# Kernel tuning notes

Measured on AMD Instinct MI355X. Metric: run time of the kernel, lower is better.

The kernel has to match this reference:

```python
import jax, jax.numpy as jnp
import numpy as np

N = 100_000   # nodes
E = 1_600_000 # edges (COO, directed as given)
D = 128       # input feature dim
H = 128       # hidden dim
L = 3         # layers


def setup_inputs() -> dict:
    key = jax.random.key(0)
    ks = jax.random.split(key, 2 + 2 * L)
    x = jax.random.normal(ks[0], (N, D), dtype=jnp.float32)
    edge_index = jax.random.randint(ks[1], (2, E), 0, N, dtype=jnp.int32)
    inp = {"x": x, "edge_index": edge_index}
    dims = [(D, H), (H, H), (H, H)]
    for i, (fi, fo) in enumerate(dims):
        scale = 1.0 / np.sqrt(fi)
        inp[f"W{i}"] = jax.random.uniform(ks[2 + 2 * i], (fi, fo), jnp.float32, -scale, scale)
        inp[f"b{i}"] = jax.random.uniform(ks[3 + 2 * i], (fo,), jnp.float32, -scale, scale)
    return inp


def reference(x, edge_index, W0, b0, W1, b1, W2, b2):
    n = x.shape[0]
    src, dst = edge_index[0], edge_index[1]
    # GCNConv default: add self-loops, symmetric D^{-1/2}(A+I)D^{-1/2} normalization
    loop = jnp.arange(n, dtype=edge_index.dtype)
    src = jnp.concatenate([src, loop])
    dst = jnp.concatenate([dst, loop])
    ones = jnp.ones(src.shape[0], dtype=x.dtype)
    deg = jax.ops.segment_sum(ones, dst, num_segments=n)          # [N]
    dinv = jnp.where(deg > 0, jax.lax.rsqrt(deg), 0.0)            # deg^{-1/2}, inf->0
    norm = dinv[src] * dinv[dst]                                  # [E+N]

    def gcn_conv(h, W, b):
        h = h @ W                                  # linear transform first (PyG order)
        msg = h[src] * norm[:, None]               # gather + scale, [E+N, H]
        return jax.ops.segment_sum(msg, dst, num_segments=n) + b

    for W, b in ((W0, b0), (W1, b1), (W2, b2)):
        x = jax.nn.relu(gcn_conv(x, W, b))
    return x
```

## Files before the change

kernel.cpp:

```cpp
#include <hip/hip_runtime.h>
#include <hip/hip_bf16.h>

#define TPB 256

typedef short s8v __attribute__((ext_vector_type(8)));
typedef float f4v __attribute__((ext_vector_type(4)));
typedef _Float16 h8v __attribute__((ext_vector_type(8)));

#define PB 128
#define BSHIFT 10
#define BSPAN 1024
#define PCHUNK 4096
#define WBLK 192

__device__ __forceinline__ unsigned short bf16_rne(float v) {
    unsigned int u = __float_as_uint(v);
    u += 0x7fffu + ((u >> 16) & 1u);
    return (unsigned short)(u >> 16);
}
__device__ __forceinline__ void split_bf16(float v, unsigned short& hi, unsigned short& lo) {
    hi = bf16_rne(v);
    float hf = __uint_as_float((unsigned int)hi << 16);
    lo = bf16_rne(v - hf);
}


__global__ __launch_bounds__(256) void bhist_wsplit_kernel(const int* __restrict__ dst, int E,
                                                           int* __restrict__ bsize,
                                                           const float* __restrict__ W0,
                                                           const float* __restrict__ W1,
                                                           const float* __restrict__ W2,
                                                           unsigned short* __restrict__ Whi,
                                                           unsigned short* __restrict__ Wlo) {
    __shared__ int h[PB];
    int t = threadIdx.x;
    if (blockIdx.x < WBLK) {
        int idx0 = blockIdx.x * 256 + t;
        if (idx0 < 3 * 16384) {
            int layer = idx0 >> 14;
            int e = idx0 & 16383;
            int k = e >> 7, ncol = e & 127;
            const float* W = (layer == 0) ? W0 : (layer == 1) ? W1 : W2;
            unsigned short hi, lo;
            split_bf16(W[e], hi, lo);
            int ct = ncol >> 4;
            int lane = (((k >> 3) & 3) << 4) | (ncol & 15);
            int kki = k >> 5;
            int j = k & 7;
            int oidx = layer * 16384 + (((ct * 4 + kki) * 64 + lane) * 8 + j);
            Whi[oidx] = hi; Wlo[oidx] = lo;
        }
        return;
    }
    int blk = blockIdx.x - WBLK;
    int nblk = gridDim.x - WBLK;
    if (t < PB) h[t] = 0;
    __syncthreads();
    for (int e = blk * 256 + t; e < E; e += nblk * 256)
        atomicAdd(&h[dst[e] >> BSHIFT], 1);
    __syncthreads();
    if (t < PB && h[t] > 0) atomicAdd(&bsize[t], h[t]);
}

__global__ void bscan_kernel(const int* __restrict__ bsize, int* __restrict__ bbase,
                             int* __restrict__ bcursor, int* __restrict__ row, int n, int E) {
    __shared__ int wtot[2];
    int t = threadIdx.x;
    int sz = bsize[t];
    int lane = t & 63, wid = t >> 6;
    int v = sz;
    for (int off = 1; off < 64; off <<= 1) {
        int u = __shfl_up(v, off);
        if (lane >= off) v += u;
    }
    if (lane == 63) wtot[wid] = v;
    __syncthreads();
    if (wid == 1) v += wtot[0];
    bbase[t + 1] = v;
    bcursor[t] = v - sz;
    if (t == 0) { bbase[0] = 0; row[n] = E; }
}

__global__ __launch_bounds__(256) void partition_kernel(const int* __restrict__ src,
                                                        const int* __restrict__ dst, int E,
                                                        int* __restrict__ bcursor,
                                                        int2* __restrict__ part) {
    __shared__ int h[PB];
    __shared__ int gofs[PB];
    int t = threadIdx.x;
    long base = (long)blockIdx.x * PCHUNK;
    int cnt = (int)min((long)PCHUNK, (long)E - base);

    if (t < PB) h[t] = 0;
    __syncthreads();
    for (int j = t; j < cnt; j += 256)
        atomicAdd(&h[dst[base + j] >> BSHIFT], 1);
    __syncthreads();
    if (t < PB) gofs[t] = (h[t] > 0) ? atomicAdd(&bcursor[t], h[t]) : 0;
    __syncthreads();
    if (t < PB) h[t] = 0;
    __syncthreads();
    for (int j = t; j < cnt; j += 256) {
        int s = src[base + j], d = dst[base + j];
        int b = d >> BSHIFT;
        int idx = atomicAdd(&h[b], 1);
        part[(long)gofs[b] + idx] = make_int2(s, d);
    }
}

__global__ __launch_bounds__(1024) void csr_kernel(const int2* __restrict__ part,
                                                   const int* __restrict__ bbase,
                                                   int* __restrict__ row, float* __restrict__ dinv,
                                                   int* __restrict__ esrc, int n) {
    __shared__ int deg[BSPAN];
    __shared__ int lrow[BSPAN];
    __shared__ int cur[BSPAN];
    __shared__ int wsum[16];
    int b = blockIdx.x;
    int n0 = b << BSHIFT;
    int nn = min(BSPAN, n - n0);
    if (nn <= 0) return;
    int e0 = bbase[b], e1 = bbase[b + 1];
    int t = threadIdx.x;

    deg[t] = 0;
    __syncthreads();
    for (int e = e0 + t; e < e1; e += 1024)
        atomicAdd(&deg[part[e].y - n0], 1);
    __syncthreads();

    int a = deg[t];
    int lane = t & 63, wid = t >> 6;
    int v = a;
    for (int off = 1; off < 64; off <<= 1) {
        int u = __shfl_up(v, off);
        if (lane >= off) v += u;
    }
    if (lane == 63) wsum[wid] = v;
    __syncthreads();
    if (wid == 0 && lane < 16) {
        int w = wsum[lane];
        for (int off = 1; off < 16; off <<= 1) {
            int u = __shfl_up(w, off);
            if (lane >= off) w += u;
        }
        wsum[lane] = w;
    }
    __syncthreads();
    int excl = v - a + ((wid > 0) ? wsum[wid - 1] : 0);
    lrow[t] = excl;
    cur[t] = 0;
    if (t < nn) {
        row[n0 + t] = e0 + excl;
        dinv[n0 + t] = rsqrtf((float)(deg[t] + 1));
    }
    __syncthreads();

    for (int e = e0 + t; e < e1; e += 1024) {
        int2 p = part[e];
        int d = p.y - n0;
        int idx = atomicAdd(&cur[d], 1);
        esrc[e0 + lrow[d] + idx] = p.x;
    }
}


__global__ __launch_bounds__(256, 3) void gemm0_mfma(const float* __restrict__ Xf,
                                                     const unsigned short* __restrict__ Whs,
                                                     const unsigned short* __restrict__ Wls,
                                                     _Float16* __restrict__ Ch, int n) {
    __shared__ _Float16 Oh[128 * 136];
    int t = threadIdx.x;
    int wave = t >> 6, lane = t & 63;
    int ch = wave & 1, rh = wave >> 1;
    int lm = lane & 15, q = lane >> 4;
    long row0 = (long)blockIdx.x * 128 + rh * 64;

    const s8v* Wh8 = (const s8v*)Whs;
    const s8v* Wl8 = (const s8v*)Wls;

    f4v acc[4][4];
#pragma unroll
    for (int rt = 0; rt < 4; rt++)
#pragma unroll
        for (int ct = 0; ct < 4; ct++) acc[rt][ct] = (f4v)0.0f;

#pragma unroll
    for (int kki = 0; kki < 4; kki++) {
        s8v bh[4], bl[4];
#pragma unroll
        for (int ct = 0; ct < 4; ct++) {
            int idx = (((ch * 4 + ct) * 4 + kki) * 64) + lane;
            bh[ct] = Wh8[idx];
            bl[ct] = Wl8[idx];
        }
        s8v ah[4], al[4];
#pragma unroll
        for (int rt = 0; rt < 4; rt++) {
            long r = row0 + rt * 16 + lm;
            long rr = (r < n) ? r : (n - 1);
            const float4* xf4 = (const float4*)(Xf + rr * 128 + kki * 32 + q * 8);
            float4 u0 = xf4[0], u1 = xf4[1];
            float uf[8] = {u0.x, u0.y, u0.z, u0.w, u1.x, u1.y, u1.z, u1.w};
            s8v hv, lv;
#pragma unroll
            for (int j = 0; j < 8; j++) {
                unsigned short hh, ll;
                split_bf16(uf[j], hh, ll);
                hv[j] = (short)hh; lv[j] = (short)ll;
            }
            ah[rt] = hv; al[rt] = lv;
        }
#pragma unroll
        for (int rt = 0; rt < 4; rt++)
#pragma unroll
            for (int ct = 0; ct < 4; ct++) {
                acc[rt][ct] = __builtin_amdgcn_mfma_f32_16x16x32_bf16(ah[rt], bh[ct], acc[rt][ct], 0, 0, 0);
                acc[rt][ct] = __builtin_amdgcn_mfma_f32_16x16x32_bf16(ah[rt], bl[ct], acc[rt][ct], 0, 0, 0);
                acc[rt][ct] = __builtin_amdgcn_mfma_f32_16x16x32_bf16(al[rt], bh[ct], acc[rt][ct], 0, 0, 0);
            }
    }

#pragma unroll
    for (int rt = 0; rt < 4; rt++)
#pragma unroll
        for (int reg = 0; reg < 4; reg++) {
            int lr = rh * 64 + rt * 16 + q * 4 + reg;
#pragma unroll
            for (int ct = 0; ct < 4; ct++)
                Oh[lr * 136 + ch * 64 + ct * 16 + lm] = (_Float16)acc[rt][ct][reg];
        }
    __syncthreads();

    long rowb = (long)blockIdx.x * 128;
    int lr = t >> 1;
    int cb = (t & 1) * 64;
    if (rowb + lr < n) {
        const uint4* s = (const uint4*)&Oh[lr * 136 + cb];
        uint4* d = (uint4*)&Ch[(rowb + lr) * 128 + cb];
#pragma unroll
        for (int u = 0; u < 8; u++) d[u] = s[u];
    }
}


__global__ __launch_bounds__(256) void fused_kernel(const h8v* __restrict__ hIn,
                                                    const float* __restrict__ dinv,
                                                    const int* __restrict__ row,
                                                    const int* __restrict__ esrc,
                                                    const float* __restrict__ bias,
                                                    const unsigned short* __restrict__ Whs,
                                                    const unsigned short* __restrict__ Wls,
                                                    _Float16* __restrict__ hOut, int n) {
    __shared__ float As[16 * 132];
    int t = threadIdx.x;
    int g = t >> 4, lane = t & 15;
    long i = (long)blockIdx.x * 16 + g;

    float r[8];
    if (i < n) {
        float di = dinv[i];
        float s2 = di * di;
        h8v self = hIn[i * 16 + lane];
        float acc[8];
#pragma unroll
        for (int k = 0; k < 8; k++) acc[k] = (float)self[k] * s2;

        int e0 = row[i], e1 = row[i + 1];
        int e = e0;
        for (; e + 4 <= e1; e += 4) {
            int s0 = esrc[e + 0];
            int s1 = esrc[e + 1];
            int s2i = esrc[e + 2];
            int s3 = esrc[e + 3];
            h8v v0 = hIn[(size_t)s0 * 16 + lane];
            h8v v1 = hIn[(size_t)s1 * 16 + lane];
            h8v v2 = hIn[(size_t)s2i * 16 + lane];
            h8v v3 = hIn[(size_t)s3 * 16 + lane];
            float w0 = dinv[s0] * di;
            float w1 = dinv[s1] * di;
            float w2 = dinv[s2i] * di;
            float w3 = dinv[s3] * di;
#pragma unroll
            for (int k = 0; k < 8; k++)
                acc[k] += w0 * (float)v0[k] + w1 * (float)v1[k] + w2 * (float)v2[k] + w3 * (float)v3[k];
        }
        for (; e < e1; ++e) {
            int s = esrc[e];
            h8v v = hIn[(size_t)s * 16 + lane];
            float w = dinv[s] * di;
#pragma unroll
            for (int k = 0; k < 8; k++) acc[k] += w * (float)v[k];
        }

        const float4* b4 = (const float4*)(bias + lane * 8);
        float4 bA = b4[0], bB = b4[1];
        r[0] = fmaxf(acc[0] + bA.x, 0.f); r[1] = fmaxf(acc[1] + bA.y, 0.f);
        r[2] = fmaxf(acc[2] + bA.z, 0.f); r[3] = fmaxf(acc[3] + bA.w, 0.f);
        r[4] = fmaxf(acc[4] + bB.x, 0.f); r[5] = fmaxf(acc[5] + bB.y, 0.f);
        r[6] = fmaxf(acc[6] + bB.z, 0.f); r[7] = fmaxf(acc[7] + bB.w, 0.f);
    } else {
#pragma unroll
        for (int k = 0; k < 8; k++) r[k] = 0.f;
    }

    float* dstA = &As[g * 132 + lane * 8];
    *(float4*)dstA = make_float4(r[0], r[1], r[2], r[3]);
    *(float4*)(dstA + 4) = make_float4(r[4], r[5], r[6], r[7]);
    __syncthreads();

    int w = t >> 6, l64 = t & 63;
    int lm = l64 & 15, q = l64 >> 4;

    const s8v* Wh8 = (const s8v*)Whs;
    const s8v* Wl8 = (const s8v*)Wls;
    s8v Bh[2][4], Bl[2][4];
#pragma unroll
    for (int c = 0; c < 2; c++)
#pragma unroll
        for (int kki = 0; kki < 4; kki++) {
            int idx = (((w * 2 + c) * 4 + kki) * 64) + l64;
            Bh[c][kki] = Wh8[idx];
            Bl[c][kki] = Wl8[idx];
        }

    f4v acc2[2];
    acc2[0] = (f4v)0.0f; acc2[1] = (f4v)0.0f;

#pragma unroll
    for (int kki = 0; kki < 4; kki++) {
        const float* ap = &As[lm * 132 + kki * 32 + q * 8];
        float4 u0 = *(const float4*)ap;
        float4 u1 = *(const float4*)(ap + 4);
        float uf[8] = {u0.x, u0.y, u0.z, u0.w, u1.x, u1.y, u1.z, u1.w};
        s8v hv, lv;
#pragma unroll
        for (int j = 0; j < 8; j++) {
            unsigned short hh, ll;
            split_bf16(uf[j], hh, ll);
            hv[j] = (short)hh; lv[j] = (short)ll;
        }
#pragma unroll
        for (int c = 0; c < 2; c++) {
            acc2[c] = __builtin_amdgcn_mfma_f32_16x16x32_bf16(hv, Bh[c][kki], acc2[c], 0, 0, 0);
            acc2[c] = __builtin_amdgcn_mfma_f32_16x16x32_bf16(hv, Bl[c][kki], acc2[c], 0, 0, 0);
            acc2[c] = __builtin_amdgcn_mfma_f32_16x16x32_bf16(lv, Bh[c][kki], acc2[c], 0, 0, 0);
        }
    }
    __syncthreads();

    _Float16* Oh = (_Float16*)As;
#pragma unroll
    for (int c = 0; c < 2; c++)
#pragma unroll
        for (int reg = 0; reg < 4; reg++)
            Oh[(q * 4 + reg) * 136 + (w * 2 + c) * 16 + lm] = (_Float16)acc2[c][reg];
    __syncthreads();

    long gi = (long)blockIdx.x * 16 + (t >> 4);
    if (gi < n) {
        uint4 v = *(const uint4*)&Oh[(t >> 4) * 136 + (t & 15) * 8];
        *(uint4*)&hOut[gi * 128 + (size_t)(t & 15) * 8] = v;
    }
}


__global__ __launch_bounds__(256) void agg_final(const h8v* __restrict__ hH,
                                                 const float* __restrict__ dinv,
                                                 const int* __restrict__ row,
                                                 const int* __restrict__ esrc,
                                                 const float* __restrict__ bias,
                                                 float* __restrict__ out, int n) {
    int g    = threadIdx.x >> 4;
    int lane = threadIdx.x & 15;
    int i = blockIdx.x * 16 + g;
    if (i >= n) return;

    float di = dinv[i];
    float s2 = di * di;

    h8v self = hH[(size_t)i * 16 + lane];
    float acc[8];
#pragma unroll
    for (int k = 0; k < 8; k++) acc[k] = (float)self[k] * s2;

    int e0 = row[i], e1 = row[i + 1];
    int e = e0;
    for (; e + 4 <= e1; e += 4) {
        int s0 = esrc[e + 0];
        int s1 = esrc[e + 1];
        int s2i = esrc[e + 2];
        int s3 = esrc[e + 3];
        h8v v0 = hH[(size_t)s0 * 16 + lane];
        h8v v1 = hH[(size_t)s1 * 16 + lane];
        h8v v2 = hH[(size_t)s2i * 16 + lane];
        h8v v3 = hH[(size_t)s3 * 16 + lane];
        float w0 = dinv[s0] * di;
        float w1 = dinv[s1] * di;
        float w2 = dinv[s2i] * di;
        float w3 = dinv[s3] * di;
#pragma unroll
        for (int k = 0; k < 8; k++)
            acc[k] += w0 * (float)v0[k] + w1 * (float)v1[k] + w2 * (float)v2[k] + w3 * (float)v3[k];
    }
    for (; e < e1; ++e) {
        int s = esrc[e];
        h8v v = hH[(size_t)s * 16 + lane];
        float w = dinv[s] * di;
#pragma unroll
        for (int k = 0; k < 8; k++) acc[k] += w * (float)v[k];
    }

    const float4* b4 = (const float4*)(bias + lane * 8);
    float4 bA = b4[0], bB = b4[1];
    float4* o4 = (float4*)(out + (size_t)i * 128 + lane * 8);
    o4[0] = make_float4(fmaxf(acc[0] + bA.x, 0.f), fmaxf(acc[1] + bA.y, 0.f),
                        fmaxf(acc[2] + bA.z, 0.f), fmaxf(acc[3] + bA.w, 0.f));
    o4[1] = make_float4(fmaxf(acc[4] + bB.x, 0.f), fmaxf(acc[5] + bB.y, 0.f),
                        fmaxf(acc[6] + bB.z, 0.f), fmaxf(acc[7] + bB.w, 0.f));
}


extern "C" void kernel_launch(void* const* d_in, const int* in_sizes, int n_in,
                              void* d_out, int out_size, void* d_ws, size_t ws_size,
                              hipStream_t stream) {
    const float* x  = (const float*)d_in[0];
    const int*   ei = (const int*)d_in[1];
    const float* W0 = (const float*)d_in[2];
    const float* b0 = (const float*)d_in[3];
    const float* W1 = (const float*)d_in[4];
    const float* b1 = (const float*)d_in[5];
    const float* W2 = (const float*)d_in[6];
    const float* b2 = (const float*)d_in[7];

    const int H = 128;
    int n = in_sizes[0] / H;
    int E = in_sizes[1] / 2;
    const int* srcp = ei;
    const int* dstp = ei + E;

    int gemm_blocks = (n + 127) / 128;
    long npad = (long)gemm_blocks * 128;
    int nbuck = (n + BSPAN - 1) >> BSHIFT;

    char* p = (char*)d_ws;
    auto alloc = [&](size_t bytes) {
        void* r = (void*)p;
        p += (bytes + 255) & ~(size_t)255;
        return r;
    };
    _Float16* bufH0 = (_Float16*)alloc((size_t)npad * H * 2);
    _Float16* bufH1 = (_Float16*)alloc((size_t)npad * H * 2);
    unsigned short* Whs = (unsigned short*)alloc(3 * 16384 * 2);
    unsigned short* Wls = (unsigned short*)alloc(3 * 16384 * 2);
    float* dinv  = (float*)alloc((size_t)n * sizeof(float));
    int*  row    = (int*)alloc((size_t)(n + 1) * sizeof(int));
    int*  bsize  = (int*)alloc(PB * sizeof(int));
    int*  bbase  = (int*)alloc((PB + 1) * sizeof(int));
    int*  bcursor= (int*)alloc(PB * sizeof(int));
    int2* part   = (int2*)alloc((size_t)E * sizeof(int2));
    int*  esrc   = (int*)alloc((size_t)E * sizeof(int));

    hipMemsetAsync(bsize, 0, PB * sizeof(int), stream);

    bhist_wsplit_kernel<<<WBLK + 1024, 256, 0, stream>>>(dstp, E, bsize, W0, W1, W2, Whs, Wls);
    bscan_kernel<<<1, PB, 0, stream>>>(bsize, bbase, bcursor, row, n, E);
    partition_kernel<<<(E + PCHUNK - 1) / PCHUNK, 256, 0, stream>>>(srcp, dstp, E, bcursor, part);
    csr_kernel<<<nbuck, 1024, 0, stream>>>(part, bbase, row, dinv, esrc, n);

    float* out = (float*)d_out;
    int node_blocks = (n + 15) / 16;

    gemm0_mfma<<<gemm_blocks, 256, 0, stream>>>(x, Whs, Wls, bufH0, n);
    fused_kernel<<<node_blocks, 256, 0, stream>>>((const h8v*)bufH0, dinv, row, esrc, b0,
                                                  Whs + 16384, Wls + 16384, bufH1, n);
    fused_kernel<<<node_blocks, 256, 0, stream>>>((const h8v*)bufH1, dinv, row, esrc, b1,
                                                  Whs + 32768, Wls + 32768, bufH0, n);
    agg_final<<<node_blocks, 256, 0, stream>>>((const h8v*)bufH0, dinv, row, esrc, b2, out, n);
}
```

Before: 404.2 us.

## Split neighbor gather across two thread groups and pack partition entries

Each node's edge list is now split between two 16-thread groups. The halves are combined through shared memory, which doubles the in-flight gathers and gives the aggregation kernels 512 threads per block. The fused MFMA stage is reworked so that each of the 8 waves computes one 16-column tile. Partition entries are packed into a single int, holding a 17-bit source index and the local destination, with 512-node buckets instead of 1024. This halves partition traffic but assumes node ids fit in 17 bits. The extra sync and LDS reduction add some overhead.

```diff
diff --git a/kernel.cpp b/kernel.cpp
--- a/kernel.cpp
+++ b/kernel.cpp
@@ -7,11 +7,12 @@
 typedef float f4v __attribute__((ext_vector_type(4)));
 typedef _Float16 h8v __attribute__((ext_vector_type(8)));
 
-#define PB 128
-#define BSHIFT 10
-#define BSPAN 1024
+#define PB 256
+#define BSHIFT 9
+#define BSPAN 512
 #define PCHUNK 4096
 #define WBLK 192
+#define SRCMASK 0x1FFFF
 
 __device__ __forceinline__ unsigned short bf16_rne(float v) {
     unsigned int u = __float_as_uint(v);
@@ -54,17 +55,17 @@
     }
     int blk = blockIdx.x - WBLK;
     int nblk = gridDim.x - WBLK;
-    if (t < PB) h[t] = 0;
+    h[t] = 0;
     __syncthreads();
     for (int e = blk * 256 + t; e < E; e += nblk * 256)
         atomicAdd(&h[dst[e] >> BSHIFT], 1);
     __syncthreads();
-    if (t < PB && h[t] > 0) atomicAdd(&bsize[t], h[t]);
+    if (h[t] > 0) atomicAdd(&bsize[t], h[t]);
 }
 
 __global__ void bscan_kernel(const int* __restrict__ bsize, int* __restrict__ bbase,
                              int* __restrict__ bcursor, int* __restrict__ row, int n, int E) {
-    __shared__ int wtot[2];
+    __shared__ int wtot[4];
     int t = threadIdx.x;
     int sz = bsize[t];
     int lane = t & 63, wid = t >> 6;
@@ -76,6 +77,8 @@
     if (lane == 63) wtot[wid] = v;
     __syncthreads();
     if (wid == 1) v += wtot[0];
+    else if (wid == 2) v += wtot[0] + wtot[1];
+    else if (wid == 3) v += wtot[0] + wtot[1] + wtot[2];
     bbase[t + 1] = v;
     bcursor[t] = v - sz;
     if (t == 0) { bbase[0] = 0; row[n] = E; }
@@ -84,38 +87,38 @@
 __global__ __launch_bounds__(256) void partition_kernel(const int* __restrict__ src,
                                                         const int* __restrict__ dst, int E,
                                                         int* __restrict__ bcursor,
-                                                        int2* __restrict__ part) {
+                                                        int* __restrict__ part) {
     __shared__ int h[PB];
     __shared__ int gofs[PB];
     int t = threadIdx.x;
     long base = (long)blockIdx.x * PCHUNK;
     int cnt = (int)min((long)PCHUNK, (long)E - base);
 
-    if (t < PB) h[t] = 0;
+    h[t] = 0;
     __syncthreads();
     for (int j = t; j < cnt; j += 256)
         atomicAdd(&h[dst[base + j] >> BSHIFT], 1);
     __syncthreads();
-    if (t < PB) gofs[t] = (h[t] > 0) ? atomicAdd(&bcursor[t], h[t]) : 0;
-    __syncthreads();
-    if (t < PB) h[t] = 0;
+    gofs[t] = (h[t] > 0) ? atomicAdd(&bcursor[t], h[t]) : 0;
+    __syncthreads();
+    h[t] = 0;
     __syncthreads();
     for (int j = t; j < cnt; j += 256) {
         int s = src[base + j], d = dst[base + j];
         int b = d >> BSHIFT;
         int idx = atomicAdd(&h[b], 1);
-        part[(long)gofs[b] + idx] = make_int2(s, d);
-    }
-}
-
-__global__ __launch_bounds__(1024) void csr_kernel(const int2* __restrict__ part,
-                                                   const int* __restrict__ bbase,
-                                                   int* __restrict__ row, float* __restrict__ dinv,
-                                                   int* __restrict__ esrc, int n) {
+        part[(long)gofs[b] + idx] = s | ((d & (BSPAN - 1)) << 17);
+    }
+}
+
+__global__ __launch_bounds__(512) void csr_kernel(const int* __restrict__ part,
+                                                  const int* __restrict__ bbase,
+                                                  int* __restrict__ row, float* __restrict__ dinv,
+                                                  int* __restrict__ esrc, int n) {
     __shared__ int deg[BSPAN];
     __shared__ int lrow[BSPAN];
     __shared__ int cur[BSPAN];
-    __shared__ int wsum[16];
+    __shared__ int wsum[8];
     int b = blockIdx.x;
     int n0 = b << BSHIFT;
     int nn = min(BSPAN, n - n0);
@@ -125,8 +128,8 @@
 
     deg[t] = 0;
     __syncthreads();
-    for (int e = e0 + t; e < e1; e += 1024)
-        atomicAdd(&deg[part[e].y - n0], 1);
+    for (int e = e0 + t; e < e1; e += 512)
+        atomicAdd(&deg[((unsigned)part[e]) >> 17], 1);
     __syncthreads();
 
     int a = deg[t];
@@ -138,9 +141,9 @@
     }
     if (lane == 63) wsum[wid] = v;
     __syncthreads();
-    if (wid == 0 && lane < 16) {
+    if (wid == 0 && lane < 8) {
         int w = wsum[lane];
-        for (int off = 1; off < 16; off <<= 1) {
+        for (int off = 1; off < 8; off <<= 1) {
             int u = __shfl_up(w, off);
             if (lane >= off) w += u;
         }
@@ -156,11 +159,11 @@
     }
     __syncthreads();
 
-    for (int e = e0 + t; e < e1; e += 1024) {
-        int2 p = part[e];
-        int d = p.y - n0;
+    for (int e = e0 + t; e < e1; e += 512) {
+        int p = part[e];
+        int d = ((unsigned)p) >> 17;
         int idx = atomicAdd(&cur[d], 1);
-        esrc[e0 + lrow[d] + idx] = p.x;
+        esrc[e0 + lrow[d] + idx] = p & SRCMASK;
     }
 }
 
@@ -244,7 +247,45 @@
 }
 
 
-__global__ __launch_bounds__(256) void fused_kernel(const h8v* __restrict__ hIn,
+__device__ __forceinline__ void gather_half(const h8v* __restrict__ hIn,
+                                            const float* __restrict__ dinv,
+                                            const int* __restrict__ row,
+                                            const int* __restrict__ esrc,
+                                            long i, float di, int half, int lane,
+                                            float acc[8]) {
+    int e0 = row[i], e1 = row[i + 1];
+    int mid = e0 + ((e1 - e0) >> 1);
+    int es = half ? mid : e0;
+    int ee = half ? e1 : mid;
+    int e = es;
+    for (; e + 4 <= ee; e += 4) {
+        int s0 = esrc[e + 0];
+        int s1 = esrc[e + 1];
+        int s2i = esrc[e + 2];
+        int s3 = esrc[e + 3];
+        h8v v0 = hIn[(size_t)s0 * 16 + lane];
+        h8v v1 = hIn[(size_t)s1 * 16 + lane];
+        h8v v2 = hIn[(size_t)s2i * 16 + lane];
+        h8v v3 = hIn[(size_t)s3 * 16 + lane];
+        float w0 = dinv[s0] * di;
+        float w1 = dinv[s1] * di;
+        float w2 = dinv[s2i] * di;
+        float w3 = dinv[s3] * di;
+#pragma unroll
+        for (int k = 0; k < 8; k++)
+            acc[k] += w0 * (float)v0[k] + w1 * (float)v1[k] + w2 * (float)v2[k] + w3 * (float)v3[k];
+    }
+    for (; e < ee; ++e) {
+        int s = esrc[e];
+        h8v v = hIn[(size_t)s * 16 + lane];
+        float w = dinv[s] * di;
+#pragma unroll
+        for (int k = 0; k < 8; k++) acc[k] += w * (float)v[k];
+    }
+}
+
+
+__global__ __launch_bounds__(512) void fused_kernel(const h8v* __restrict__ hIn,
                                                     const float* __restrict__ dinv,
                                                     const int* __restrict__ row,
                                                     const int* __restrict__ esrc,
@@ -253,60 +294,48 @@
                                                     const unsigned short* __restrict__ Wls,
                                                     _Float16* __restrict__ hOut, int n) {
     __shared__ float As[16 * 132];
-    int t = threadIdx.x;
-    int g = t >> 4, lane = t & 15;
-    long i = (long)blockIdx.x * 16 + g;
-
-    float r[8];
+    __shared__ float Bs[16 * 132];
+    int t = threadIdx.x;
+    int grp = t >> 4, lane = t & 15;
+    int g2 = grp >> 1, half = grp & 1;
+    long i = (long)blockIdx.x * 16 + g2;
+
+    float acc[8];
+#pragma unroll
+    for (int k = 0; k < 8; k++) acc[k] = 0.f;
+    float di = 0.f;
     if (i < n) {
-        float di = dinv[i];
+        di = dinv[i];
+        gather_half(hIn, dinv, row, esrc, i, di, half, lane, acc);
+    }
+    if (half) {
+        float* d = &Bs[g2 * 132 + lane * 8];
+        *(float4*)d = make_float4(acc[0], acc[1], acc[2], acc[3]);
+        *(float4*)(d + 4) = make_float4(acc[4], acc[5], acc[6], acc[7]);
+    }
+    __syncthreads();
+    if (!half) {
+        float r[8];
+        const float* o = &Bs[g2 * 132 + lane * 8];
+        float4 oa = *(const float4*)o, ob = *(const float4*)(o + 4);
+        float oth[8] = {oa.x, oa.y, oa.z, oa.w, ob.x, ob.y, ob.z, ob.w};
         float s2 = di * di;
-        h8v self = hIn[i * 16 + lane];
-        float acc[8];
-#pragma unroll
-        for (int k = 0; k < 8; k++) acc[k] = (float)self[k] * s2;
-
-        int e0 = row[i], e1 = row[i + 1];
-        int e = e0;
-        for (; e + 4 <= e1; e += 4) {
-            int s0 = esrc[e + 0];
-            int s1 = esrc[e + 1];
-            int s2i = esrc[e + 2];
-            int s3 = esrc[e + 3];
-            h8v v0 = hIn[(size_t)s0 * 16 + lane];
-            h8v v1 = hIn[(size_t)s1 * 16 + lane];
-            h8v v2 = hIn[(size_t)s2i * 16 + lane];
-            h8v v3 = hIn[(size_t)s3 * 16 + lane];
-            float w0 = dinv[s0] * di;
-            float w1 = dinv[s1] * di;
-            float w2 = dinv[s2i] * di;
-            float w3 = dinv[s3] * di;
-#pragma unroll
-            for (int k = 0; k < 8; k++)
-                acc[k] += w0 * (float)v0[k] + w1 * (float)v1[k] + w2 * (float)v2[k] + w3 * (float)v3[k];
-        }
-        for (; e < e1; ++e) {
-            int s = esrc[e];
-            h8v v = hIn[(size_t)s * 16 + lane];
-            float w = dinv[s] * di;
-#pragma unroll
-            for (int k = 0; k < 8; k++) acc[k] += w * (float)v[k];
-        }
-
         const float4* b4 = (const float4*)(bias + lane * 8);
         float4 bA = b4[0], bB = b4[1];
-        r[0] = fmaxf(acc[0] + bA.x, 0.f); r[1] = fmaxf(acc[1] + bA.y, 0.f);
-        r[2] = fmaxf(acc[2] + bA.z, 0.f); r[3] = fmaxf(acc[3] + bA.w, 0.f);
-        r[4] = fmaxf(acc[4] + bB.x, 0.f); r[5] = fmaxf(acc[5] + bB.y, 0.f);
-        r[6] = fmaxf(acc[6] + bB.z, 0.f); r[7] = fmaxf(acc[7] + bB.w, 0.f);
-    } else {
-#pragma unroll
-        for (int k = 0; k < 8; k++) r[k] = 0.f;
-    }
-
-    float* dstA = &As[g * 132 + lane * 8];
-    *(float4*)dstA = make_float4(r[0], r[1], r[2], r[3]);
-    *(float4*)(dstA + 4) = make_float4(r[4], r[5], r[6], r[7]);
+        float bb[8] = {bA.x, bA.y, bA.z, bA.w, bB.x, bB.y, bB.z, bB.w};
+        if (i < n) {
+            h8v self = hIn[i * 16 + lane];
+#pragma unroll
+            for (int k = 0; k < 8; k++)
+                r[k] = fmaxf(acc[k] + oth[k] + (float)self[k] * s2 + bb[k], 0.f);
+        } else {
+#pragma unroll
+            for (int k = 0; k < 8; k++) r[k] = 0.f;
+        }
+        float* dstA = &As[g2 * 132 + lane * 8];
+        *(float4*)dstA = make_float4(r[0], r[1], r[2], r[3]);
+        *(float4*)(dstA + 4) = make_float4(r[4], r[5], r[6], r[7]);
+    }
     __syncthreads();
 
     int w = t >> 6, l64 = t & 63;
@@ -314,19 +343,15 @@
 
     const s8v* Wh8 = (const s8v*)Whs;
     const s8v* Wl8 = (const s8v*)Wls;
-    s8v Bh[2][4], Bl[2][4];
-#pragma unroll
-    for (int c = 0; c < 2; c++)
-#pragma unroll
-        for (int kki = 0; kki < 4; kki++) {
-            int idx = (((w * 2 + c) * 4 + kki) * 64) + l64;
-            Bh[c][kki] = Wh8[idx];
-            Bl[c][kki] = Wl8[idx];
-        }
-
-    f4v acc2[2];
-    acc2[0] = (f4v)0.0f; acc2[1] = (f4v)0.0f;
-
+    s8v Bh[4], Bl[4];
+#pragma unroll
+    for (int kki = 0; kki < 4; kki++) {
+        int idx = ((w * 4 + kki) * 64) + l64;
+        Bh[kki] = Wh8[idx];
+        Bl[kki] = Wl8[idx];
+    }
+
+    f4v a2 = (f4v)0.0f;
 #pragma unroll
     for (int kki = 0; kki < 4; kki++) {
         const float* ap = &As[lm * 132 + kki * 32 + q * 8];
@@ -340,84 +365,71 @@
             split_bf16(uf[j], hh, ll);
             hv[j] = (short)hh; lv[j] = (short)ll;
         }
-#pragma unroll
-        for (int c = 0; c < 2; c++) {
-            acc2[c] = __builtin_amdgcn_mfma_f32_16x16x32_bf16(hv, Bh[c][kki], acc2[c], 0, 0, 0);
-            acc2[c] = __builtin_amdgcn_mfma_f32_16x16x32_bf16(hv, Bl[c][kki], acc2[c], 0, 0, 0);
-            acc2[c] = __builtin_amdgcn_mfma_f32_16x16x32_bf16(lv, Bh[c][kki], acc2[c], 0, 0, 0);
-        }
+        a2 = __builtin_amdgcn_mfma_f32_16x16x32_bf16(hv, Bh[kki], a2, 0, 0, 0);
+        a2 = __builtin_amdgcn_mfma_f32_16x16x32_bf16(hv, Bl[kki], a2, 0, 0, 0);
+        a2 = __builtin_amdgcn_mfma_f32_16x16x32_bf16(lv, Bh[kki], a2, 0, 0, 0);
     }
     __syncthreads();
 
     _Float16* Oh = (_Float16*)As;
 #pragma unroll
-    for (int c = 0; c < 2; c++)
-#pragma unroll
-        for (int reg = 0; reg < 4; reg++)
-            Oh[(q * 4 + reg) * 136 + (w * 2 + c) * 16 + lm] = (_Float16)acc2[c][reg];
-    __syncthreads();
-
-    long gi = (long)blockIdx.x * 16 + (t >> 4);
-    if (gi < n) {
-        uint4 v = *(const uint4*)&Oh[(t >> 4) * 136 + (t & 15) * 8];
-        *(uint4*)&hOut[gi * 128 + (size_t)(t & 15) * 8] = v;
-    }
-}
-
-
-__global__ __launch_bounds__(256) void agg_final(const h8v* __restrict__ hH,
+    for (int reg = 0; reg < 4; reg++)
+        Oh[(q * 4 + reg) * 136 + w * 16 + lm] = (_Float16)a2[reg];
+    __syncthreads();
+
+    if (t < 256) {
+        long gi = (long)blockIdx.x * 16 + (t >> 4);
+        if (gi < n) {
+            uint4 v = *(const uint4*)&Oh[(t >> 4) * 136 + (t & 15) * 8];
+            *(uint4*)&hOut[gi * 128 + (size_t)(t & 15) * 8] = v;
+        }
+    }
+}
+
+
+__global__ __launch_bounds__(512) void agg_final(const h8v* __restrict__ hH,
                                                  const float* __restrict__ dinv,
                                                  const int* __restrict__ row,
                                                  const int* __restrict__ esrc,
                                                  const float* __restrict__ bias,
                                                  float* __restrict__ out, int n) {
-    int g    = threadIdx.x >> 4;
-    int lane = threadIdx.x & 15;
-    int i = blockIdx.x * 16 + g;
-    if (i >= n) return;
-
-    float di = dinv[i];
-    float s2 = di * di;
-
-    h8v self = hH[(size_t)i * 16 + lane];
+    __shared__ float Bs[16 * 132];
+    int t = threadIdx.x;
+    int grp = t >> 4, lane = t & 15;
+    int g2 = grp >> 1, half = grp & 1;
+    long i = (long)blockIdx.x * 16 + g2;
+
     float acc[8];
 #pragma unroll
-    for (int k = 0; k < 8; k++) acc[k] = (float)self[k] * s2;
-
-    int e0 = row[i], e1 = row[i + 1];
-    int e = e0;
-    for (; e + 4 <= e1; e += 4) {
-        int s0 = esrc[e + 0];
-        int s1 = esrc[e + 1];
-        int s2i = esrc[e + 2];
-        int s3 = esrc[e + 3];
-        h8v v0 = hH[(size_t)s0 * 16 + lane];
-        h8v v1 = hH[(size_t)s1 * 16 + lane];
-        h8v v2 = hH[(size_t)s2i * 16 + lane];
-        h8v v3 = hH[(size_t)s3 * 16 + lane];
-        float w0 = dinv[s0] * di;
-        float w1 = dinv[s1] * di;
-        float w2 = dinv[s2i] * di;
-        float w3 = dinv[s3] * di;
+    for (int k = 0; k < 8; k++) acc[k] = 0.f;
+    float di = 0.f;
+    if (i < n) {
+        di = dinv[i];
+        gather_half(hH, dinv, row, esrc, i, di, half, lane, acc);
+    }
+    if (half) {
+        float* d = &Bs[g2 * 132 + lane * 8];
+        *(float4*)d = make_float4(acc[0], acc[1], acc[2], acc[3]);
+        *(float4*)(d + 4) = make_float4(acc[4], acc[5], acc[6], acc[7]);
+    }
+    __syncthreads();
+    if (!half && i < n) {
+        const float* o = &Bs[g2 * 132 + lane * 8];
+        float4 oa = *(const float4*)o, ob = *(const float4*)(o + 4);
+        float oth[8] = {oa.x, oa.y, oa.z, oa.w, ob.x, ob.y, ob.z, ob.w};
+        float s2 = di * di;
+        h8v self = hH[i * 16 + lane];
+        const float4* b4 = (const float4*)(bias + lane * 8);
+        float4 bA = b4[0], bB = b4[1];
+        float bb[8] = {bA.x, bA.y, bA.z, bA.w, bB.x, bB.y, bB.z, bB.w};
+        float r[8];
 #pragma unroll
         for (int k = 0; k < 8; k++)
-            acc[k] += w0 * (float)v0[k] + w1 * (float)v1[k] + w2 * (float)v2[k] + w3 * (float)v3[k];
-    }
-    for (; e < e1; ++e) {
-        int s = esrc[e];
-        h8v v = hH[(size_t)s * 16 + lane];
-        float w = dinv[s] * di;
-#pragma unroll
-        for (int k = 0; k < 8; k++) acc[k] += w * (float)v[k];
-    }
-
-    const float4* b4 = (const float4*)(bias + lane * 8);
-    float4 bA = b4[0], bB = b4[1];
-    float4* o4 = (float4*)(out + (size_t)i * 128 + lane * 8);
-    o4[0] = make_float4(fmaxf(acc[0] + bA.x, 0.f), fmaxf(acc[1] + bA.y, 0.f),
-                        fmaxf(acc[2] + bA.z, 0.f), fmaxf(acc[3] + bA.w, 0.f));
-    o4[1] = make_float4(fmaxf(acc[4] + bB.x, 0.f), fmaxf(acc[5] + bB.y, 0.f),
-                        fmaxf(acc[6] + bB.z, 0.f), fmaxf(acc[7] + bB.w, 0.f));
+            r[k] = fmaxf(acc[k] + oth[k] + (float)self[k] * s2 + bb[k], 0.f);
+        float4* o4 = (float4*)(out + i * 128 + lane * 8);
+        o4[0] = make_float4(r[0], r[1], r[2], r[3]);
+        o4[1] = make_float4(r[4], r[5], r[6], r[7]);
+    }
 }
 
 
@@ -458,7 +470,7 @@
     int*  bsize  = (int*)alloc(PB * sizeof(int));
     int*  bbase  = (int*)alloc((PB + 1) * sizeof(int));
     int*  bcursor= (int*)alloc(PB * sizeof(int));
-    int2* part   = (int2*)alloc((size_t)E * sizeof(int2));
+    int*  part   = (int*)alloc((size_t)E * sizeof(int));
     int*  esrc   = (int*)alloc((size_t)E * sizeof(int));
 
     hipMemsetAsync(bsize, 0, PB * sizeof(int), stream);
@@ -466,15 +478,15 @@
     bhist_wsplit_kernel<<<WBLK + 1024, 256, 0, stream>>>(dstp, E, bsize, W0, W1, W2, Whs, Wls);
     bscan_kernel<<<1, PB, 0, stream>>>(bsize, bbase, bcursor, row, n, E);
     partition_kernel<<<(E + PCHUNK - 1) / PCHUNK, 256, 0, stream>>>(srcp, dstp, E, bcursor, part);
-    csr_kernel<<<nbuck, 1024, 0, stream>>>(part, bbase, row, dinv, esrc, n);
+    csr_kernel<<<nbuck, 512, 0, stream>>>(part, bbase, row, dinv, esrc, n);
 
     float* out = (float*)d_out;
     int node_blocks = (n + 15) / 16;
 
     gemm0_mfma<<<gemm_blocks, 256, 0, stream>>>(x, Whs, Wls, bufH0, n);
-    fused_kernel<<<node_blocks, 256, 0, stream>>>((const h8v*)bufH0, dinv, row, esrc, b0,
+    fused_kernel<<<node_blocks, 512, 0, stream>>>((const h8v*)bufH0, dinv, row, esrc, b0,
                                                   Whs + 16384, Wls + 16384, bufH1, n);
-    fused_kernel<<<node_blocks, 256, 0, stream>>>((const h8v*)bufH1, dinv, row, esrc, b1,
+    fused_kernel<<<node_blocks, 512, 0, stream>>>((const h8v*)bufH1, dinv, row, esrc, b1,
                                                   Whs + 32768, Wls + 32768, bufH0, n);
-    agg_final<<<node_blocks, 256, 0, stream>>>((const h8v*)bufH0, dinv, row, esrc, b2, out, n);
-}
+    agg_final<<<node_blocks, 512, 0, stream>>>((const h8v*)bufH0, dinv, row, esrc, b2, out, n);
+}
```

New measurement: 411.8 us. No clear change (+1.9%).
